# Kernel tuning notes

Hardware: AMD Instinct MI355X
Metric: run time of the kernel (lower is better)

## Reference

```python
import jax, jax.numpy as jnp
import numpy as np

H = 50   # hidden_size
D = 8    # input_size
B = 2048
T = 512


def setup_inputs() -> dict:
    key = jax.random.key(0)
    ks = jax.random.split(key, 11)
    s = 1.0 / np.sqrt(H)  # PyTorch LSTM/Linear default init bound
    u = lambda k, shape: jax.random.uniform(k, shape, jnp.float32, -s, s)
    return {
        "x": jax.random.normal(ks[0], (B, T, D), jnp.float32),
        # layer 0: input 8 -> hidden 50 (gate order i,f,g,o as in PyTorch)
        "Wih0": u(ks[1], (4 * H, D)),
        "Whh0": u(ks[2], (4 * H, H)),
        "bih0": u(ks[3], (4 * H,)),
        "bhh0": u(ks[4], (4 * H,)),
        # layer 1: hidden 50 -> hidden 50
        "Wih1": u(ks[5], (4 * H, H)),
        "Whh1": u(ks[6], (4 * H, H)),
        "bih1": u(ks[7], (4 * H,)),
        "bhh1": u(ks[8], (4 * H,)),
        # final linear 50 -> 1
        "Wlin": u(ks[9], (1, H)),
        "blin": u(ks[10], (1,)),
    }


def _lstm_layer(x, Wih, Whh, b):
    # x: [B, T, Din] -> outputs h over time: [B, T, H]
    Bb = x.shape[0]
    Hh = Whh.shape[1]
    # precompute input-to-gate projection for all timesteps (one big GEMM)
    x_proj = jnp.einsum("btd,gd->btg", x, Wih) + b  # [B, T, 4H]

    def step(carry, xt):
        h, c = carry
        gates = xt + h @ Whh.T  # [B, 4H]
        i, f, g, o = jnp.split(gates, 4, axis=-1)
        i = jax.nn.sigmoid(i)
        f = jax.nn.sigmoid(f)
        g = jnp.tanh(g)
        o = jax.nn.sigmoid(o)
        c = f * c + i * g
        h = o * jnp.tanh(c)
        return (h, c), h

    init = (jnp.zeros((Bb, Hh), x.dtype), jnp.zeros((Bb, Hh), x.dtype))
    _, hs = jax.lax.scan(step, init, jnp.swapaxes(x_proj, 0, 1))  # [T, B, H]
    return jnp.swapaxes(hs, 0, 1)


def reference(x, Wih0, Whh0, bih0, bhh0, Wih1, Whh1, bih1, bhh1, Wlin, blin):
    h1 = _lstm_layer(x, Wih0, Whh0, bih0 + bhh0)   # [B, T, H]
    h2 = _lstm_layer(h1, Wih1, Whh1, bih1 + bhh1)  # [B, T, H]
    last = h2[:, -1, :]                            # [B, H]
    return last @ Wlin.T + blin                    # [B, 1]
```

## Files before the change

kernel.cpp:

```cpp
#include <hip/hip_runtime.h>
#include <math.h>

#define Hn 50
#define Dn 8
#define Tn 512
#define BB 8
#define NBLK 256
#define KST 136

typedef __attribute__((ext_vector_type(8))) short short8;
typedef __attribute__((ext_vector_type(4))) float f32x4;

__device__ __forceinline__ float fexp2_(float x) {
#if __has_builtin(__builtin_amdgcn_exp2f)
    return __builtin_amdgcn_exp2f(x);
#else
    return exp2f(x);
#endif
}
__device__ __forceinline__ float frcp_(float x) {
#if __has_builtin(__builtin_amdgcn_rcpf)
    return __builtin_amdgcn_rcpf(x);
#else
    return 1.0f / x;
#endif
}
__device__ __forceinline__ float sigmoidf_(float x) {
    return frcp_(1.0f + fexp2_(-1.44269504f * x));
}
__device__ __forceinline__ float tanhf_(float x) {
    return 2.0f * sigmoidf_(2.0f * x) - 1.0f;
}
__device__ __forceinline__ float bf2f(short s) {
    return __uint_as_float(((unsigned)(unsigned short)s) << 16);
}
__device__ __forceinline__ void split_bf(float v, short& hi, short& lo) {
    hi = (short)(__float_as_uint(v) >> 16);
    const float r = v - bf2f(hi);
    lo = (short)(__float_as_uint(r) >> 16);
}
__device__ __forceinline__ float lstm_cell4(const f32x4 g4, float& c) {
    c = sigmoidf_(g4.y) * c + sigmoidf_(g4.x) * tanhf_(g4.z);
    return sigmoidf_(g4.w) * tanhf_(c);
}
__device__ __forceinline__ float shflxor8(float v) {
    return __shfl_xor(v, 8, 64);
}


template<int NL1, int NL0, bool XD>
__device__ __forceinline__ void run_loop(
    const int* l1T, const int* l0T,
    int b0, int lane, int quad, int col,
    short (*bP)[16][KST], float* h1f, const float* x,
    const float* Wih0, const float* Whh0, const float* bih0, const float* bhh0,
    const float* Wih1, const float* Whh1, const float* bih1, const float* bhh1)
{
    constexpr int NS = NL1 + NL0;
    constexpr int NPAIR = (NS + 1) / 2;
    constexpr int NBF = (NL1 > 0) ? 4 : 2;

    short8 W1[NL1 > 0 ? NL1 : 1][4][2];
    short8 W0[NL0 > 0 ? NL0 : 1][2][2];
    float  bias[NS][4];
    int    kb[NS];
    int    cellb[NS];

    #pragma unroll
    for (int i = 0; i < NL1; ++i) {
        const int T = l1T[i];
        const int ng = T * 16 + col, cl = ng >> 2, g = ng & 3;
        const bool on = (cl < Hn);
        const int grow = g * Hn + cl;
        #pragma unroll
        for (int s = 0; s < 4; ++s)
            #pragma unroll
            for (int j = 0; j < 8; ++j) {
                const int k = 32 * s + quad * 8 + j;
                float v = 0.f;
                if (on) {
                    if (k < Hn)                      v = Wih1[grow * Hn + k];
                    else if (k >= 64 && k < 64 + Hn) v = Whh1[grow * Hn + (k - 64)];
                }
                short hi, lo; split_bf(v, hi, lo);
                W1[i][s][0][j] = hi; W1[i][s][1][j] = lo;
            }
        const int myc = 4 * T + quad;
        #pragma unroll
        for (int r = 0; r < 4; ++r)
            bias[i][r] = (myc < Hn) ? (bih1[r * Hn + myc] + bhh1[r * Hn + myc]) : 0.f;
        kb[i] = 64 + 4 * T; cellb[i] = 4 * T;
    }
    #pragma unroll
    for (int i = 0; i < NL0; ++i) {
        const int T = l0T[i];
        const int ng = T * 16 + col, cl = ng >> 2, g = ng & 3;
        const bool on = (cl < Hn);
        const int grow = g * Hn + cl;
        #pragma unroll
        for (int s = 0; s < 2; ++s)
            #pragma unroll
            for (int j = 0; j < 8; ++j) {
                const int k = 32 * s + quad * 8 + j;
                float v = 0.f;
                if (on) {
                    if (k < Hn)           v = Whh0[grow * Hn + k];
                    else if (k < Hn + Dn) v = Wih0[grow * Dn + (k - Hn)];
                }
                short hi, lo; split_bf(v, hi, lo);
                W0[i][s][0][j] = hi; W0[i][s][1][j] = lo;
            }
        const int myc = 4 * T + quad;
        #pragma unroll
        for (int r = 0; r < 4; ++r)
            bias[NL1 + i][r] = (myc < Hn) ? (bih0[r * Hn + myc] + bhh0[r * Hn + myc]) : 0.f;
        kb[NL1 + i] = 4 * T; cellb[NL1 + i] = 4 * T;
    }

    float c[NPAIR];
    #pragma unroll
    for (int p = 0; p < NPAIR; ++p) c[p] = 0.f;

    const float* xp = XD ? (x + (size_t)(b0 + (lane >> 3)) * Tn * Dn + (lane & 7))
                         : (const float*)nullptr;

    for (int t = 0; t < Tn; ++t) {
        float xv = 0.f;
        if (XD) { if (t + 1 < Tn) xv = xp[(size_t)(t + 1) * Dn]; }

        const short (*bR)[KST] = (const short (*)[KST])bP[t & 1];
        short (*bW)[KST] = bP[(t + 1) & 1];

        short8 BF[NBF];
        #pragma unroll
        for (int s = 0; s < NBF; ++s)
            BF[s] = *(const short8*)&bR[col][32 * s + quad * 8];

        f32x4 acc[NS];
        #pragma unroll
        for (int i = 0; i < NS; ++i) {
            #pragma unroll
            for (int r = 0; r < 4; ++r) acc[i][r] = (col < 8) ? bias[i][r] : 0.f;
        }
        #pragma unroll
        for (int i = 0; i < NL1; ++i)
            #pragma unroll
            for (int s = 0; s < 4; ++s) {
                acc[i] = __builtin_amdgcn_mfma_f32_16x16x32_bf16(W1[i][s][0], BF[s], acc[i], 0, 0, 0);
                acc[i] = __builtin_amdgcn_mfma_f32_16x16x32_bf16(W1[i][s][1], BF[s], acc[i], 0, 0, 0);
            }
        #pragma unroll
        for (int i = 0; i < NL0; ++i)
            #pragma unroll
            for (int s = 0; s < 2; ++s) {
                acc[NL1 + i] = __builtin_amdgcn_mfma_f32_16x16x32_bf16(W0[i][s][0], BF[s], acc[NL1 + i], 0, 0, 0);
                acc[NL1 + i] = __builtin_amdgcn_mfma_f32_16x16x32_bf16(W0[i][s][1], BF[s], acc[NL1 + i], 0, 0, 0);
            }

        #pragma unroll
        for (int p = 0; p < NPAIR; ++p) {
            const int ia = 2 * p;
            const bool hasB  = (ia + 1 < NS);
            const bool isL1a = (ia < NL1);
            const bool isL1b = (ia + 1 < NL1);
            f32x4 g;
            #pragma unroll
            for (int r = 0; r < 4; ++r) {
                if (hasB) {
                    const float u = (col < 8) ? acc[ia][r]     : acc[ia + 1][r];
                    const float v = (col < 8) ? acc[ia + 1][r] : acc[ia][r];
                    g[r] = u + shflxor8(v);
                } else {
                    g[r] = acc[ia][r] + shflxor8(acc[ia][r]);
                }
            }
            int cell, kc; bool isl1;
            if (hasB && col >= 8) { cell = cellb[ia + 1] + quad; kc = kb[ia + 1] + quad; isl1 = isL1b; }
            else                  { cell = cellb[ia] + quad;     kc = kb[ia] + quad;     isl1 = isL1a; }
            const bool doAct = (cell < Hn) && ((t >= 1) || !isl1);
            if (doAct) {
                const float h = lstm_cell4(g, c[p]);
                short hi, lo; split_bf(h, hi, lo);
                if (hasB) { bW[col & 7][kc] = hi; bW[(col & 7) + 8][kc] = lo; }
                else      { bW[col][kc] = (col < 8) ? hi : lo; }
            }
        }
        if (XD) {
            if (t + 1 < Tn) {
                short hi, lo; split_bf(xv, hi, lo);
                bW[lane >> 3][Hn + (lane & 7)]       = hi;
                bW[(lane >> 3) + 8][Hn + (lane & 7)] = lo;
            }
        }
        __syncthreads();
    }

    if constexpr (NL1 > 0) {
        const short (*bR)[KST] = (const short (*)[KST])bP[Tn & 1];
        short8 BF[4];
        #pragma unroll
        for (int s = 0; s < 4; ++s)
            BF[s] = *(const short8*)&bR[col][32 * s + quad * 8];
        f32x4 accE[NL1];
        #pragma unroll
        for (int i = 0; i < NL1; ++i) {
            #pragma unroll
            for (int r = 0; r < 4; ++r) accE[i][r] = (col < 8) ? bias[i][r] : 0.f;
        }
        #pragma unroll
        for (int i = 0; i < NL1; ++i)
            #pragma unroll
            for (int s = 0; s < 4; ++s) {
                accE[i] = __builtin_amdgcn_mfma_f32_16x16x32_bf16(W1[i][s][0], BF[s], accE[i], 0, 0, 0);
                accE[i] = __builtin_amdgcn_mfma_f32_16x16x32_bf16(W1[i][s][1], BF[s], accE[i], 0, 0, 0);
            }
        #pragma unroll
        for (int p = 0; p < NPAIR; ++p) {
            const int ia = 2 * p;
            if (ia < NL1) {
                const bool bL1 = (ia + 1 < NL1);
                f32x4 g;
                #pragma unroll
                for (int r = 0; r < 4; ++r) {
                    if (bL1) {
                        const float u = (col < 8) ? accE[ia][r]     : accE[ia + 1][r];
                        const float v = (col < 8) ? accE[ia + 1][r] : accE[ia][r];
                        g[r] = u + shflxor8(v);
                    } else {
                        g[r] = accE[ia][r] + shflxor8(accE[ia][r]);
                    }
                }
                int cell; bool mine;
                if (bL1) { cell = ((col < 8) ? cellb[ia] : cellb[ia + 1]) + quad; mine = true; }
                else     { cell = cellb[ia] + quad;                               mine = (col < 8); }
                if (mine && cell < Hn) {
                    const float h = lstm_cell4(g, c[p]);
                    h1f[cell * 8 + (col & 7)] = h;
                }
            }
        }
    }
}

__global__ __launch_bounds__(512, 2) void lstm2_kernel(
    const float* __restrict__ x,
    const float* __restrict__ Wih0, const float* __restrict__ Whh0,
    const float* __restrict__ bih0, const float* __restrict__ bhh0,
    const float* __restrict__ Wih1, const float* __restrict__ Whh1,
    const float* __restrict__ bih1, const float* __restrict__ bhh1,
    const float* __restrict__ Wlin, const float* __restrict__ blin,
    float* __restrict__ out)
{
    const int tid  = threadIdx.x;
    const int b0   = blockIdx.x * BB;
    const int w    = __builtin_amdgcn_readfirstlane(tid >> 6);
    const int lane = tid & 63;
    const int quad = lane >> 4;
    const int col  = lane & 15;

    __shared__ __align__(16) short bP[2][16][KST];
    __shared__ float h1f[Hn * 8];

    for (int i = tid; i < 2 * 16 * KST; i += 512) (&bP[0][0][0])[i] = 0;
    __syncthreads();
    if (tid < 64) {
        const int xb = tid >> 3, xd = tid & 7;
        const float f = x[((size_t)(b0 + xb) * Tn + 0) * Dn + xd];
        short hi, lo; split_bf(f, hi, lo);
        bP[0][xb][Hn + xd]     = hi;
        bP[0][xb + 8][Hn + xd] = lo;
    }
    __syncthreads();

    if (w == 0) {
        const int l0t[4] = {0, 1, 2, 3};
        run_loop<0, 4, false>(nullptr, l0t, b0, lane, quad, col, bP, h1f, x,
                              Wih0, Whh0, bih0, bhh0, Wih1, Whh1, bih1, bhh1);
    } else if (w == 1) {
        const int l0t[3] = {4, 5, 6};
        run_loop<0, 3, false>(nullptr, l0t, b0, lane, quad, col, bP, h1f, x,
                              Wih0, Whh0, bih0, bhh0, Wih1, Whh1, bih1, bhh1);
    } else if (w == 2) {
        const int l0t[3] = {7, 8, 9};
        run_loop<0, 3, false>(nullptr, l0t, b0, lane, quad, col, bP, h1f, x,
                              Wih0, Whh0, bih0, bhh0, Wih1, Whh1, bih1, bhh1);
    } else if (w == 3) {
        const int l0t[3] = {10, 11, 12};
        run_loop<0, 3, true>(nullptr, l0t, b0, lane, quad, col, bP, h1f, x,
                             Wih0, Whh0, bih0, bhh0, Wih1, Whh1, bih1, bhh1);
    } else if (w == 7) {
        const int l1t[4] = {9, 10, 11, 12};
        run_loop<4, 0, false>(l1t, nullptr, b0, lane, quad, col, bP, h1f, x,
                              Wih0, Whh0, bih0, bhh0, Wih1, Whh1, bih1, bhh1);
    } else {
        const int l1t[3] = {3 * (w - 4), 3 * (w - 4) + 1, 3 * (w - 4) + 2};
        run_loop<3, 0, false>(l1t, nullptr, b0, lane, quad, col, bP, h1f, x,
                              Wih0, Whh0, bih0, bhh0, Wih1, Whh1, bih1, bhh1);
    }
    __syncthreads();

    if (tid < BB) {
        float o = blin[0];
        #pragma unroll
        for (int k = 0; k < Hn; ++k) o += Wlin[k] * h1f[k * 8 + tid];
        out[b0 + tid] = o;
    }
}

extern "C" void kernel_launch(void* const* d_in, const int* in_sizes, int n_in,
                              void* d_out, int out_size, void* d_ws, size_t ws_size,
                              hipStream_t stream) {
    const float* x    = (const float*)d_in[0];
    const float* Wih0 = (const float*)d_in[1];
    const float* Whh0 = (const float*)d_in[2];
    const float* bih0 = (const float*)d_in[3];
    const float* bhh0 = (const float*)d_in[4];
    const float* Wih1 = (const float*)d_in[5];
    const float* Whh1 = (const float*)d_in[6];
    const float* bih1 = (const float*)d_in[7];
    const float* bhh1 = (const float*)d_in[8];
    const float* Wlin = (const float*)d_in[9];
    const float* blin = (const float*)d_in[10];
    float* out = (float*)d_out;

    lstm2_kernel<<<NBLK, 512, 0, stream>>>(x, Wih0, Whh0, bih0, bhh0,
                                           Wih1, Whh1, bih1, bhh1,
                                           Wlin, blin, out);
}
```

Measured before the change: 471.1 us.

## Spread gate tiles over sixteen waves per block and precompute LDS offsets

After: 427.6 us. 1.1x faster.

```diff
diff --git a/kernel.cpp b/kernel.cpp
--- a/kernel.cpp
+++ b/kernel.cpp
@@ -62,7 +62,7 @@
 
     short8 W1[NL1 > 0 ? NL1 : 1][4][2];
     short8 W0[NL0 > 0 ? NL0 : 1][2][2];
-    float  bias[NS][4];
+    f32x4  biasv[NS];
     int    kb[NS];
     int    cellb[NS];
 
@@ -88,7 +88,8 @@
         const int myc = 4 * T + quad;
         #pragma unroll
         for (int r = 0; r < 4; ++r)
-            bias[i][r] = (myc < Hn) ? (bih1[r * Hn + myc] + bhh1[r * Hn + myc]) : 0.f;
+            biasv[i][r] = ((myc < Hn) && (col < 8))
+                        ? (bih1[r * Hn + myc] + bhh1[r * Hn + myc]) : 0.f;
         kb[i] = 64 + 4 * T; cellb[i] = 4 * T;
     }
     #pragma unroll
@@ -113,8 +114,31 @@
         const int myc = 4 * T + quad;
         #pragma unroll
         for (int r = 0; r < 4; ++r)
-            bias[NL1 + i][r] = (myc < Hn) ? (bih0[r * Hn + myc] + bhh0[r * Hn + myc]) : 0.f;
+            biasv[NL1 + i][r] = ((myc < Hn) && (col < 8))
+                              ? (bih0[r * Hn + myc] + bhh0[r * Hn + myc]) : 0.f;
         kb[NL1 + i] = 4 * T; cellb[NL1 + i] = 4 * T;
+    }
+
+    const short* base0 = &bP[0][0][0];
+    const short* base1 = &bP[1][0][0];
+    int rdo[NBF];
+    #pragma unroll
+    for (int s = 0; s < NBF; ++s) rdo[s] = col * KST + 32 * s + quad * 8;
+
+    int  wofH[NPAIR], wofL[NPAIR], wofS[NPAIR];
+    bool actOK[NPAIR], lagged[NPAIR];
+    #pragma unroll
+    for (int p = 0; p < NPAIR; ++p) {
+        const int ia = 2 * p;
+        const bool hasB = (ia + 1 < NS);
+        const int slot = (hasB && col >= 8) ? ia + 1 : ia;
+        const int cell = cellb[slot] + quad;
+        const int kc   = kb[slot] + quad;
+        lagged[p] = (slot < NL1);
+        actOK[p]  = (cell < Hn);
+        wofH[p] = (col & 7) * KST + kc;
+        wofL[p] = wofH[p] + 8 * KST;
+        wofS[p] = col * KST + kc;
     }
 
     float c[NPAIR];
@@ -128,20 +152,17 @@
         float xv = 0.f;
         if (XD) { if (t + 1 < Tn) xv = xp[(size_t)(t + 1) * Dn]; }
 
-        const short (*bR)[KST] = (const short (*)[KST])bP[t & 1];
-        short (*bW)[KST] = bP[(t + 1) & 1];
+        const short* rb = (t & 1) ? base1 : base0;
+        short* wb = (short*)((t & 1) ? base0 : base1);
 
         short8 BF[NBF];
         #pragma unroll
         for (int s = 0; s < NBF; ++s)
-            BF[s] = *(const short8*)&bR[col][32 * s + quad * 8];
+            BF[s] = *(const short8*)&rb[rdo[s]];
 
         f32x4 acc[NS];
         #pragma unroll
-        for (int i = 0; i < NS; ++i) {
-            #pragma unroll
-            for (int r = 0; r < 4; ++r) acc[i][r] = (col < 8) ? bias[i][r] : 0.f;
-        }
+        for (int i = 0; i < NS; ++i) acc[i] = biasv[i];
         #pragma unroll
         for (int i = 0; i < NL1; ++i)
             #pragma unroll
@@ -160,9 +181,7 @@
         #pragma unroll
         for (int p = 0; p < NPAIR; ++p) {
             const int ia = 2 * p;
-            const bool hasB  = (ia + 1 < NS);
-            const bool isL1a = (ia < NL1);
-            const bool isL1b = (ia + 1 < NL1);
+            const bool hasB = (ia + 1 < NS);
             f32x4 g;
             #pragma unroll
             for (int r = 0; r < 4; ++r) {
@@ -174,39 +193,33 @@
                     g[r] = acc[ia][r] + shflxor8(acc[ia][r]);
                 }
             }
-            int cell, kc; bool isl1;
-            if (hasB && col >= 8) { cell = cellb[ia + 1] + quad; kc = kb[ia + 1] + quad; isl1 = isL1b; }
-            else                  { cell = cellb[ia] + quad;     kc = kb[ia] + quad;     isl1 = isL1a; }
-            const bool doAct = (cell < Hn) && ((t >= 1) || !isl1);
+            const bool doAct = actOK[p] && ((t >= 1) || !lagged[p]);
             if (doAct) {
                 const float h = lstm_cell4(g, c[p]);
                 short hi, lo; split_bf(h, hi, lo);
-                if (hasB) { bW[col & 7][kc] = hi; bW[(col & 7) + 8][kc] = lo; }
-                else      { bW[col][kc] = (col < 8) ? hi : lo; }
+                if (hasB) { wb[wofH[p]] = hi; wb[wofL[p]] = lo; }
+                else      { wb[wofS[p]] = (col < 8) ? hi : lo; }
             }
         }
         if (XD) {
             if (t + 1 < Tn) {
                 short hi, lo; split_bf(xv, hi, lo);
-                bW[lane >> 3][Hn + (lane & 7)]       = hi;
-                bW[(lane >> 3) + 8][Hn + (lane & 7)] = lo;
+                wb[(lane >> 3) * KST + Hn + (lane & 7)]       = hi;
+                wb[((lane >> 3) + 8) * KST + Hn + (lane & 7)] = lo;
             }
         }
         __syncthreads();
     }
 
     if constexpr (NL1 > 0) {
-        const short (*bR)[KST] = (const short (*)[KST])bP[Tn & 1];
+        const short* rb = base0;
         short8 BF[4];
         #pragma unroll
         for (int s = 0; s < 4; ++s)
-            BF[s] = *(const short8*)&bR[col][32 * s + quad * 8];
+            BF[s] = *(const short8*)&rb[col * KST + 32 * s + quad * 8];
         f32x4 accE[NL1];
         #pragma unroll
-        for (int i = 0; i < NL1; ++i) {
-            #pragma unroll
-            for (int r = 0; r < 4; ++r) accE[i][r] = (col < 8) ? bias[i][r] : 0.f;
-        }
+        for (int i = 0; i < NL1; ++i) accE[i] = biasv[i];
         #pragma unroll
         for (int i = 0; i < NL1; ++i)
             #pragma unroll
@@ -242,7 +255,7 @@
     }
 }
 
-__global__ __launch_bounds__(512, 2) void lstm2_kernel(
+__global__ __launch_bounds__(1024) void lstm2_kernel(
     const float* __restrict__ x,
     const float* __restrict__ Wih0, const float* __restrict__ Whh0,
     const float* __restrict__ bih0, const float* __restrict__ bhh0,
@@ -261,7 +274,7 @@
     __shared__ __align__(16) short bP[2][16][KST];
     __shared__ float h1f[Hn * 8];
 
-    for (int i = tid; i < 2 * 16 * KST; i += 512) (&bP[0][0][0])[i] = 0;
+    for (int i = tid; i < 2 * 16 * KST; i += 1024) (&bP[0][0][0])[i] = 0;
     __syncthreads();
     if (tid < 64) {
         const int xb = tid >> 3, xd = tid & 7;
@@ -272,30 +285,27 @@
     }
     __syncthreads();
 
-    if (w == 0) {
-        const int l0t[4] = {0, 1, 2, 3};
-        run_loop<0, 4, false>(nullptr, l0t, b0, lane, quad, col, bP, h1f, x,
+    if (w < 8) {
+        const int l1t[1] = {w};
+        const int l0t[1] = {w};
+        run_loop<1, 1, false>(l1t, l0t, b0, lane, quad, col, bP, h1f, x,
                               Wih0, Whh0, bih0, bhh0, Wih1, Whh1, bih1, bhh1);
-    } else if (w == 1) {
-        const int l0t[3] = {4, 5, 6};
-        run_loop<0, 3, false>(nullptr, l0t, b0, lane, quad, col, bP, h1f, x,
+    } else if (w < 13) {
+        const int l1t[1] = {w};
+        run_loop<1, 0, false>(l1t, nullptr, b0, lane, quad, col, bP, h1f, x,
                               Wih0, Whh0, bih0, bhh0, Wih1, Whh1, bih1, bhh1);
-    } else if (w == 2) {
-        const int l0t[3] = {7, 8, 9};
-        run_loop<0, 3, false>(nullptr, l0t, b0, lane, quad, col, bP, h1f, x,
+    } else if (w == 13) {
+        const int l0t[2] = {8, 9};
+        run_loop<0, 2, false>(nullptr, l0t, b0, lane, quad, col, bP, h1f, x,
                               Wih0, Whh0, bih0, bhh0, Wih1, Whh1, bih1, bhh1);
-    } else if (w == 3) {
-        const int l0t[3] = {10, 11, 12};
-        run_loop<0, 3, true>(nullptr, l0t, b0, lane, quad, col, bP, h1f, x,
-                             Wih0, Whh0, bih0, bhh0, Wih1, Whh1, bih1, bhh1);
-    } else if (w == 7) {
-        const int l1t[4] = {9, 10, 11, 12};
-        run_loop<4, 0, false>(l1t, nullptr, b0, lane, quad, col, bP, h1f, x,
+    } else if (w == 14) {
+        const int l0t[2] = {10, 11};
+        run_loop<0, 2, false>(nullptr, l0t, b0, lane, quad, col, bP, h1f, x,
                               Wih0, Whh0, bih0, bhh0, Wih1, Whh1, bih1, bhh1);
     } else {
-        const int l1t[3] = {3 * (w - 4), 3 * (w - 4) + 1, 3 * (w - 4) + 2};
-        run_loop<3, 0, false>(l1t, nullptr, b0, lane, quad, col, bP, h1f, x,
-                              Wih0, Whh0, bih0, bhh0, Wih1, Whh1, bih1, bhh1);
+        const int l0t[1] = {12};
+        run_loop<0, 1, true>(nullptr, l0t, b0, lane, quad, col, bP, h1f, x,
+                             Wih0, Whh0, bih0, bhh0, Wih1, Whh1, bih1, bhh1);
     }
     __syncthreads();
 
@@ -323,7 +333,7 @@
     const float* blin = (const float*)d_in[10];
     float* out = (float*)d_out;
 
-    lstm2_kernel<<<NBLK, 512, 0, stream>>>(x, Wih0, Whh0, bih0, bhh0,
-                                           Wih1, Whh1, bih1, bhh1,
-                                           Wlin, blin, out);
-}
+    lstm2_kernel<<<NBLK, 1024, 0, stream>>>(x, Wih0, Whh0, bih0, bhh0,
+                                            Wih1, Whh1, bih1, bhh1,
+                                            Wlin, blin, out);
+}
```
